# Optimization experiments

Measured on AMD Instinct MI355X. Metric: run time of the kernel, lower is better.

## Reference

```python
import jax, jax.numpy as jnp
import numpy as np

NUM_NODES = 100000
OUT_CHANNELS = 32
NUM_EDGES = 3200000


def setup_inputs() -> dict:
    key = jax.random.key(0)
    k1, k2, k3 = jax.random.split(key, 3)
    edge_index = jax.random.randint(k1, (2, NUM_EDGES), 0, NUM_NODES, dtype=jnp.int64)
    # nn.Linear init: weight [out, in], uniform(-1/sqrt(in), 1/sqrt(in))
    bound = 1.0 / np.sqrt(NUM_NODES)
    W = jax.random.uniform(k2, (OUT_CHANNELS, NUM_NODES), jnp.float32, -bound, bound)
    b = jax.random.uniform(k3, (OUT_CHANNELS,), jnp.float32, -bound, bound)
    return {"edge_index": edge_index, "W": W, "b": b}


def reference(edge_index, W, b):
    # LINK forward: A = sparse COO [N, num_nodes] with 1.0 per edge (duplicates sum),
    # logits = A @ W.T + b. Implemented as gather + segment_sum (no dense A).
    row = edge_index[0]
    col = edge_index[1]
    row = row - row.min()  # faithful to `row = row - row.min()`
    gathered = jnp.take(W.T, col, axis=0)  # [E, out_channels]
    logits = jax.ops.segment_sum(gathered, row, num_segments=NUM_NODES)  # [N, out]
    return logits + b
```

## Files before the change

### kernel.cpp

```cpp
#include <hip/hip_runtime.h>

#define NUM_NODES 100000
#define OUT_CH 32
#define NUM_EDGES 3200000

#define RPB 128
#define NB 782
#define CAP2 5120
#define TPB 512
#define TILE 12800
#define KPT 25
#define NTILE 250

__global__ void init_kernel(int* __restrict__ bcount, int* __restrict__ ws_min) {
    int i = blockIdx.x * blockDim.x + threadIdx.x;
    if (i < NB) bcount[i] = 0;
    if (i == 0) *ws_min = 0x7fffffff;
}

__global__ void min_kernel(const int4* __restrict__ row4, int* __restrict__ ws_min) {
    int tid = blockIdx.x * blockDim.x + threadIdx.x;
    int stride = gridDim.x * blockDim.x;
    int m = 0x7fffffff;
    for (int i = tid; i < NUM_EDGES / 4; i += stride) {
        int4 v = row4[i];
        m = min(m, min(min(v.x, v.y), min(v.z, v.w)));
    }
    #pragma unroll
    for (int off = 32; off > 0; off >>= 1) m = min(m, __shfl_down(m, off, 64));
    if ((threadIdx.x & 63) == 0) atomicMin(ws_min, m);
}

__global__ void transpose_kernel(const float* __restrict__ W, float* __restrict__ Wt) {
    __shared__ float tile[32][33];
    int tx = threadIdx.x;
    int c  = threadIdx.y;
    int colBase = blockIdx.x * 32;
    tile[c][tx] = W[c * NUM_NODES + colBase + tx];
    __syncthreads();
    Wt[(colBase + c) * 32 + tx] = tile[tx][c];
}

__global__ void __launch_bounds__(TPB)
bin_stage(const int* __restrict__ edge, const int* __restrict__ ws_min,
          int* __restrict__ bcount, unsigned int* __restrict__ bin) {
    __shared__ int cnt[NB];
    __shared__ int cur[NB];
    int t = threadIdx.x;
    int eb = blockIdx.x * TILE;
    int rmin = *ws_min;
    for (int i = t; i < NB; i += TPB) cnt[i] = 0;
    __syncthreads();

    unsigned int ent[KPT];
    int bb[KPT];
    #pragma unroll
    for (int k = 0; k < KPT; k++) {
        int e = eb + k * TPB + t;
        int r = edge[e] - rmin;
        int c = edge[NUM_EDGES + e];
        int b = r >> 7;
        bb[k]  = b;
        ent[k] = ((unsigned int)(r & 127) << 17) | (unsigned int)c;
        atomicAdd(&cnt[b], 1);
    }
    __syncthreads();

    for (int i = t; i < NB; i += TPB) cur[i] = cnt[i] ? atomicAdd(&bcount[i], cnt[i]) : 0;
    __syncthreads();

    #pragma unroll
    for (int k = 0; k < KPT; k++) {
        int pos = atomicAdd(&cur[bb[k]], 1);
        if (pos < CAP2) bin[(size_t)bb[k] * CAP2 + pos] = ent[k];
    }
}

__global__ void __launch_bounds__(TPB)
bucket_gather(const unsigned int* __restrict__ bin, const int* __restrict__ bcount,
              const float* __restrict__ Wt, const float* __restrict__ b,
              float* __restrict__ out) {
    __shared__ int cnt2[RPB * 8];
    __shared__ int cur2[RPB * 8];
    __shared__ int rowstart[RPB];
    __shared__ int rowcnt[RPB];
    __shared__ int scn[RPB];
    __shared__ int lcol[CAP2];

    int t = threadIdx.x;
    int bk = blockIdx.x;
    int n = bcount[bk];
    if (n > CAP2) n = CAP2;
    const unsigned int* mybin = bin + (size_t)bk * CAP2;

    for (int i = t; i < RPB * 8; i += TPB) cnt2[i] = 0;
    __syncthreads();

    for (int i = t; i < n; i += TPB) {
        unsigned int p = mybin[i];
        int lr  = p >> 17;
        int seg = (p & 0x1FFFF) >> 14;
        atomicAdd(&cnt2[(lr << 3) | seg], 1);
    }
    __syncthreads();

    if (t < RPB) {
        int s = 0;
        #pragma unroll
        for (int k = 0; k < 8; k++) s += cnt2[(t << 3) | k];
        rowcnt[t] = s;
        scn[t] = s;
    }
    __syncthreads();
    for (int off = 1; off < RPB; off <<= 1) {
        int v = (t < RPB && t >= off) ? scn[t - off] : 0;
        __syncthreads();
        if (t < RPB) scn[t] += v;
        __syncthreads();
    }
    if (t < RPB) {
        int rs = scn[t] - rowcnt[t];
        rowstart[t] = rs;
        int run = rs;
        #pragma unroll
        for (int k = 0; k < 8; k++) { cur2[(t << 3) | k] = run; run += cnt2[(t << 3) | k]; }
    }
    __syncthreads();

    for (int i = t; i < n; i += TPB) {
        unsigned int p = mybin[i];
        int lr = p >> 17;
        int c  = p & 0x1FFFF;
        int pos = atomicAdd(&cur2[(lr << 3) | (c >> 14)], 1);
        lcol[pos] = c;
    }
    __syncthreads();

    int g   = t >> 3;
    int sub = t & 7;
    float4 bias = ((const float4*)b)[sub];
    const float4* Wt4 = (const float4*)Wt;
    for (int lr = g; lr < RPB; lr += 64) {
        int row = bk * RPB + lr;
        if (row >= NUM_NODES) break;
        int s = rowstart[lr];
        int e = s + rowcnt[lr];
        float4 acc = bias;
        for (int i = s; i < e; i++) {
            float4 w = Wt4[lcol[i] * 8 + sub];
            acc.x += w.x; acc.y += w.y; acc.z += w.z; acc.w += w.w;
        }
        ((float4*)out)[(size_t)row * 8 + sub] = acc;
    }
}

extern "C" void kernel_launch(void* const* d_in, const int* in_sizes, int n_in,
                              void* d_out, int out_size, void* d_ws, size_t ws_size,
                              hipStream_t stream) {
    const int*   edge = (const int*)d_in[0];
    const float* W    = (const float*)d_in[1];
    const float* b    = (const float*)d_in[2];
    float* out = (float*)d_out;

    char* ws = (char*)d_ws;
    int*          ws_min = (int*)ws;
    int*          bcount = (int*)(ws + 256);
    float*        Wt     = (float*)(ws + 4096);
    unsigned int* bin    = (unsigned int*)(ws + 12845056);

    init_kernel<<<(NB + 255) / 256, 256, 0, stream>>>(bcount, ws_min);
    min_kernel<<<256, 256, 0, stream>>>((const int4*)edge, ws_min);
    transpose_kernel<<<NUM_NODES / 32, dim3(32, 32), 0, stream>>>(W, Wt);
    bin_stage<<<NTILE, TPB, 0, stream>>>(edge, ws_min, bcount, bin);
    bucket_gather<<<NB, TPB, 0, stream>>>(bin, bcount, Wt, b, out);
}
```

Before: 173.8 us.

## Fuse init, min-reduction and transpose into one kernel; unroll gather accumulation

Result: faster. 161.3 us (-7.2%).

```diff
diff --git a/kernel.cpp b/kernel.cpp
--- a/kernel.cpp
+++ b/kernel.cpp
@@ -11,46 +11,67 @@
 #define TILE 12800
 #define KPT 25
 #define NTILE 250
-
-__global__ void init_kernel(int* __restrict__ bcount, int* __restrict__ ws_min) {
-    int i = blockIdx.x * blockDim.x + threadIdx.x;
-    if (i < NB) bcount[i] = 0;
-    if (i == 0) *ws_min = 0x7fffffff;
-}
-
-__global__ void min_kernel(const int4* __restrict__ row4, int* __restrict__ ws_min) {
-    int tid = blockIdx.x * blockDim.x + threadIdx.x;
-    int stride = gridDim.x * blockDim.x;
-    int m = 0x7fffffff;
-    for (int i = tid; i < NUM_EDGES / 4; i += stride) {
-        int4 v = row4[i];
-        m = min(m, min(min(v.x, v.y), min(v.z, v.w)));
-    }
-    #pragma unroll
-    for (int off = 32; off > 0; off >>= 1) m = min(m, __shfl_down(m, off, 64));
-    if ((threadIdx.x & 63) == 0) atomicMin(ws_min, m);
-}
-
-__global__ void transpose_kernel(const float* __restrict__ W, float* __restrict__ Wt) {
-    __shared__ float tile[32][33];
-    int tx = threadIdx.x;
-    int c  = threadIdx.y;
-    int colBase = blockIdx.x * 32;
-    tile[c][tx] = W[c * NUM_NODES + colBase + tx];
-    __syncthreads();
-    Wt[(colBase + c) * 32 + tx] = tile[tx][c];
+#define TR_BLOCKS 3125
+#define MIN_BLOCKS 256
+
+__global__ void __launch_bounds__(256)
+fused_pre(const float* __restrict__ W, float* __restrict__ Wt,
+          const int4* __restrict__ row4, int* __restrict__ partmin,
+          int* __restrict__ bcount) {
+    int bk = blockIdx.x;
+    int t  = threadIdx.x;
+    if (bk < TR_BLOCKS) {
+        __shared__ float tile[32][33];
+        int tx = t & 31, ty = t >> 5;
+        int colBase = bk * 32;
+        #pragma unroll
+        for (int k = 0; k < 4; k++) {
+            int c = ty + 8 * k;
+            tile[c][tx] = W[c * NUM_NODES + colBase + tx];
+        }
+        __syncthreads();
+        #pragma unroll
+        for (int k = 0; k < 4; k++) {
+            int c = ty + 8 * k;
+            Wt[(colBase + c) * 32 + tx] = tile[tx][c];
+        }
+    } else if (bk < TR_BLOCKS + MIN_BLOCKS) {
+        int mb  = bk - TR_BLOCKS;
+        int tid = mb * 256 + t;
+        int m = 0x7fffffff;
+        for (int i = tid; i < NUM_EDGES / 4; i += MIN_BLOCKS * 256) {
+            int4 v = row4[i];
+            m = min(m, min(min(v.x, v.y), min(v.z, v.w)));
+        }
+        #pragma unroll
+        for (int off = 32; off > 0; off >>= 1) m = min(m, __shfl_down(m, off, 64));
+        __shared__ int wm[4];
+        if ((t & 63) == 0) wm[t >> 6] = m;
+        __syncthreads();
+        if (t == 0) partmin[mb] = min(min(wm[0], wm[1]), min(wm[2], wm[3]));
+    } else {
+        for (int i = t; i < NB; i += 256) bcount[i] = 0;
+    }
 }
 
 __global__ void __launch_bounds__(TPB)
-bin_stage(const int* __restrict__ edge, const int* __restrict__ ws_min,
+bin_stage(const int* __restrict__ edge, const int* __restrict__ partmin,
           int* __restrict__ bcount, unsigned int* __restrict__ bin) {
     __shared__ int cnt[NB];
     __shared__ int cur[NB];
+    __shared__ int rminS;
     int t = threadIdx.x;
+    if (t < 64) {
+        int m = min(min(partmin[t], partmin[t + 64]),
+                    min(partmin[t + 128], partmin[t + 192]));
+        #pragma unroll
+        for (int off = 32; off > 0; off >>= 1) m = min(m, __shfl_down(m, off, 64));
+        if (t == 0) rminS = m;
+    }
+    for (int i = t; i < NB; i += TPB) cnt[i] = 0;
+    __syncthreads();
+    int rmin = rminS;
     int eb = blockIdx.x * TILE;
-    int rmin = *ws_min;
-    for (int i = t; i < NB; i += TPB) cnt[i] = 0;
-    __syncthreads();
 
     unsigned int ent[KPT];
     int bb[KPT];
@@ -145,11 +166,30 @@
         if (row >= NUM_NODES) break;
         int s = rowstart[lr];
         int e = s + rowcnt[lr];
-        float4 acc = bias;
-        for (int i = s; i < e; i++) {
+        float4 a0 = bias;
+        float4 a1 = make_float4(0.f, 0.f, 0.f, 0.f);
+        float4 a2 = make_float4(0.f, 0.f, 0.f, 0.f);
+        float4 a3 = make_float4(0.f, 0.f, 0.f, 0.f);
+        int i = s;
+        for (; i + 4 <= e; i += 4) {
+            float4 w0 = Wt4[lcol[i]     * 8 + sub];
+            float4 w1 = Wt4[lcol[i + 1] * 8 + sub];
+            float4 w2 = Wt4[lcol[i + 2] * 8 + sub];
+            float4 w3 = Wt4[lcol[i + 3] * 8 + sub];
+            a0.x += w0.x; a0.y += w0.y; a0.z += w0.z; a0.w += w0.w;
+            a1.x += w1.x; a1.y += w1.y; a1.z += w1.z; a1.w += w1.w;
+            a2.x += w2.x; a2.y += w2.y; a2.z += w2.z; a2.w += w2.w;
+            a3.x += w3.x; a3.y += w3.y; a3.z += w3.z; a3.w += w3.w;
+        }
+        for (; i < e; i++) {
             float4 w = Wt4[lcol[i] * 8 + sub];
-            acc.x += w.x; acc.y += w.y; acc.z += w.z; acc.w += w.w;
-        }
+            a0.x += w.x; a0.y += w.y; a0.z += w.z; a0.w += w.w;
+        }
+        float4 acc;
+        acc.x = (a0.x + a1.x) + (a2.x + a3.x);
+        acc.y = (a0.y + a1.y) + (a2.y + a3.y);
+        acc.z = (a0.z + a1.z) + (a2.z + a3.z);
+        acc.w = (a0.w + a1.w) + (a2.w + a3.w);
         ((float4*)out)[(size_t)row * 8 + sub] = acc;
     }
 }
@@ -163,14 +203,12 @@
     float* out = (float*)d_out;
 
     char* ws = (char*)d_ws;
-    int*          ws_min = (int*)ws;
-    int*          bcount = (int*)(ws + 256);
-    float*        Wt     = (float*)(ws + 4096);
-    unsigned int* bin    = (unsigned int*)(ws + 12845056);
-
-    init_kernel<<<(NB + 255) / 256, 256, 0, stream>>>(bcount, ws_min);
-    min_kernel<<<256, 256, 0, stream>>>((const int4*)edge, ws_min);
-    transpose_kernel<<<NUM_NODES / 32, dim3(32, 32), 0, stream>>>(W, Wt);
-    bin_stage<<<NTILE, TPB, 0, stream>>>(edge, ws_min, bcount, bin);
+    int*          partmin = (int*)ws;
+    int*          bcount  = (int*)(ws + 1024);
+    float*        Wt      = (float*)(ws + 8192);
+    unsigned int* bin     = (unsigned int*)(ws + 12845056);
+
+    fused_pre<<<TR_BLOCKS + MIN_BLOCKS + 1, 256, 0, stream>>>(W, Wt, (const int4*)edge, partmin, bcount);
+    bin_stage<<<NTILE, TPB, 0, stream>>>(edge, partmin, bcount, bin);
     bucket_gather<<<NB, TPB, 0, stream>>>(bin, bcount, Wt, b, out);
 }
```
